# Optimization experiments

Hardware: AMD Instinct MI355X
Metric: run time of the kernel (lower is better)

The kernel has to match this reference:

```python
import jax, jax.numpy as jnp
import numpy as np

V, E, H, B, S = 32000, 128, 256, 8, 512


def setup_inputs() -> dict:
    key = jax.random.key(0)
    ks = jax.random.split(key, 8)
    s_cell = 1.0 / np.sqrt(H)
    return {
        "t": jax.random.randint(ks[0], (B, S), 0, V),
        "emb": jax.random.normal(ks[1], (V, E), dtype=jnp.float32) * 0.02,
        "h0": jnp.zeros((1, H), dtype=jnp.float32),
        "w_ih": jax.random.uniform(ks[2], (3 * H, E), jnp.float32, -s_cell, s_cell),
        "w_hh": jax.random.uniform(ks[3], (3 * H, H), jnp.float32, -s_cell, s_cell),
        "b_ih": jax.random.uniform(ks[4], (3 * H,), jnp.float32, -s_cell, s_cell),
        "b_hh": jax.random.uniform(ks[5], (3 * H,), jnp.float32, -s_cell, s_cell),
        "w_out": jax.random.normal(ks[6], (V, H), dtype=jnp.float32) * 0.02,
        "b_out": jnp.zeros((V,), dtype=jnp.float32),
    }


def reference(t, emb, h0, w_ih, w_hh, b_ih, b_hh, w_out, b_out):
    x = emb[t]  # [B, S, E]
    # Input-side gate pre-activations can be batched over time (same math as per-step GRUCell)
    gi = jnp.einsum("bse,ge->bsg", x, w_ih) + b_ih  # [B, S, 3H]
    h_init = jnp.broadcast_to(h0, (t.shape[0], h0.shape[1]))  # [B, H]

    def step(h, gi_t):  # gi_t: [B, 3H]
        gh = h @ w_hh.T + b_hh  # [B, 3H]
        i_r, i_z, i_n = jnp.split(gi_t, 3, axis=-1)
        h_r, h_z, h_n = jnp.split(gh, 3, axis=-1)
        r = jax.nn.sigmoid(i_r + h_r)
        z = jax.nn.sigmoid(i_z + h_z)
        n = jnp.tanh(i_n + r * h_n)
        h_new = (1.0 - z) * n + z * h
        return h_new, h_new

    _, hs = jax.lax.scan(step, h_init, jnp.swapaxes(gi, 0, 1))  # hs: [S, B, H]
    hidden = jnp.swapaxes(hs, 0, 1)  # [B, S, H]
    return jnp.einsum("bsh,vh->bsv", hidden, w_out) + b_out  # [B, S, V]
```

## Files before the change

kernel.cpp:

```cpp
#include <hip/hip_runtime.h>
#include <stdint.h>


typedef __attribute__((ext_vector_type(8))) _Float16 half8;
typedef __attribute__((ext_vector_type(4))) _Float16 half4;
typedef __attribute__((ext_vector_type(4))) float float4v;
typedef __attribute__((ext_vector_type(4))) float facc4;
typedef __attribute__((ext_vector_type(4))) unsigned short ushort4v;

#define GI_BYTES   (512 * 8 * 768 * 4)
#define HID_BYTES  (4096 * 256 * 2)
#define FLAG_OFF   (GI_BYTES + HID_BYTES)

__device__ __forceinline__ float b2f(unsigned short u) {
  union { unsigned int i; float f; } v; v.i = ((unsigned int)u) << 16; return v.f;
}
__device__ __forceinline__ unsigned short f2b(float f) {
  union { float f; unsigned int i; } v; v.f = f;
  unsigned int r = v.i + 0x7FFFu + ((v.i >> 16) & 1u);
  return (unsigned short)(r >> 16);
}
template<bool BF> __device__ __forceinline__ float ldf(const void* p, int i) {
  if constexpr (BF) return b2f(((const unsigned short*)p)[i]);
  else              return ((const float*)p)[i];
}
template<bool BF> __device__ __forceinline__ float4v ld4(const void* p, int i) {
  float4v r;
  if constexpr (BF) {
    ushort4v u = *reinterpret_cast<const ushort4v*>((const unsigned short*)p + i);
#pragma unroll
    for (int j = 0; j < 4; ++j) r[j] = b2f(u[j]);
  } else {
    r = *reinterpret_cast<const float4v*>((const float*)p + i);
  }
  return r;
}

__global__ void k_detect(const unsigned int* __restrict__ emb_raw,
                         int* __restrict__ flag) {
  int tid = threadIdx.x;
  unsigned int u = emb_raw[tid];
  unsigned int lo = u & 0xFFFFu;
  unsigned int ex = (lo >> 7) & 0xFFu;
  int hit = ((ex >= 96u && ex <= 127u) || lo == 0u) ? 1 : 0;
  unsigned long long m = __ballot(hit);
  if (tid == 0) flag[0] = (__popcll(m) >= 40) ? 1 : 0;
}

template<bool BF>
__global__ __launch_bounds__(256, 4) void k_gi(
    const int* __restrict__ flag, const int* __restrict__ t,
    const void* __restrict__ emb, const void* __restrict__ w_ih,
    const void* __restrict__ b_ih, float* __restrict__ gi)
{
  if (*flag != (BF ? 1 : 0)) return;
  alignas(16) __shared__ float x_lds[4][128];
  const int n0 = blockIdx.x * 4;
  const int tid = threadIdx.x;
  for (int i = tid; i < 512; i += 256) {
    int tk = i >> 7, e = i & 127;
    int n = n0 + tk, s = n >> 3, b = n & 7;
    int tok = t[b * 512 + s];
    x_lds[tk][e] = ldf<BF>(emb, tok * 128 + e);
  }
  __syncthreads();
#pragma unroll
  for (int gg = 0; gg < 3; ++gg) {
    int g = gg * 256 + tid;
    float bias = ldf<BF>(b_ih, g);
    float a0 = bias, a1 = bias, a2 = bias, a3 = bias;
    for (int kb = 0; kb < 32; ++kb) {
      float4v w4 = ld4<BF>(w_ih, g * 128 + kb * 4);
#pragma unroll
      for (int j = 0; j < 4; ++j) {
        float w = w4[j]; int k = kb * 4 + j;
        a0 = fmaf(w, x_lds[0][k], a0);
        a1 = fmaf(w, x_lds[1][k], a1);
        a2 = fmaf(w, x_lds[2][k], a2);
        a3 = fmaf(w, x_lds[3][k], a3);
      }
    }
    gi[(n0 + 0) * 768 + g] = a0;
    gi[(n0 + 1) * 768 + g] = a1;
    gi[(n0 + 2) * 768 + g] = a2;
    gi[(n0 + 3) * 768 + g] = a3;
  }
}

template<bool BF>
__global__ __launch_bounds__(512, 2) void k_scan(
    const int* __restrict__ flag, const void* __restrict__ w_hh,
    const void* __restrict__ b_hh, const void* __restrict__ h0,
    const float* __restrict__ gi, _Float16* __restrict__ hidden)
{
  if (*flag != (BF ? 1 : 0)) return;
  alignas(16) __shared__ _Float16 a_lds[4096];
  alignas(16) __shared__ float gh_lds[8 * 772];
  alignas(16) __shared__ float bhh_lds[768];

  const int tid = threadIdx.x;
  const int wave = tid >> 6, lane = tid & 63;
  const int l15 = lane & 15, q = lane >> 4;
  const int b = tid & 7, jb = tid >> 3, j0 = jb * 4;
  const int kt0 = jb >> 3, q0 = (jb >> 1) & 3, off0 = (jb & 1) * 4;

  half8 bfr[6][8];
#pragma unroll
  for (int tt = 0; tt < 6; ++tt) {
    int nrow = wave * 96 + tt * 16 + l15;
#pragma unroll
    for (int kt = 0; kt < 8; ++kt) {
      int base = nrow * 256 + kt * 32 + q * 8;
      float4v x0 = ld4<BF>(w_hh, base), x1 = ld4<BF>(w_hh, base + 4);
      half8 h;
#pragma unroll
      for (int j = 0; j < 4; ++j) { h[j] = (_Float16)x0[j]; h[4 + j] = (_Float16)x1[j]; }
      bfr[tt][kt] = h;
    }
  }

  for (int i = tid; i < 4096; i += 512) a_lds[i] = (_Float16)0.f;
  for (int i = tid; i < 768; i += 512) bhh_lds[i] = ldf<BF>(b_hh, i);
  __syncthreads();

  float hreg[4];
  {
    float4v h04 = ld4<BF>(h0, j0);
    half4 h4;
#pragma unroll
    for (int i = 0; i < 4; ++i) { hreg[i] = h04[i]; h4[i] = (_Float16)h04[i]; }
    *reinterpret_cast<half4*>(&a_lds[kt0 * 512 + (q0 * 16 + b) * 8 + off0]) = h4;
  }
  __syncthreads();

  for (int s = 0; s < 512; ++s) {
    facc4 acc[6] = {};
#pragma unroll
    for (int kt = 0; kt < 8; ++kt) {
      half8 a = *reinterpret_cast<const half8*>(&a_lds[kt * 512 + lane * 8]);
#pragma unroll
      for (int tt = 0; tt < 6; ++tt)
        acc[tt] = __builtin_amdgcn_mfma_f32_16x16x32_f16(a, bfr[tt][kt],
                                                         acc[tt], 0, 0, 0);
    }
    const float* gis = gi + s * 6144 + b * 768 + j0;
    float4v g_r = *reinterpret_cast<const float4v*>(gis);
    float4v g_z = *reinterpret_cast<const float4v*>(gis + 256);
    float4v g_n = *reinterpret_cast<const float4v*>(gis + 512);
    if (q < 2) {
#pragma unroll
      for (int tt = 0; tt < 6; ++tt) {
        int nrow = wave * 96 + tt * 16 + l15;
#pragma unroll
        for (int i = 0; i < 4; ++i)
          gh_lds[(q * 4 + i) * 772 + nrow] = acc[tt][i] + bhh_lds[nrow];
      }
    }
    __syncthreads();

    const float* ghb = gh_lds + b * 772;
    half4 hb;
#pragma unroll
    for (int i = 0; i < 4; ++i) {
      int j = j0 + i;
      float r = 1.f / (1.f + __expf(-(g_r[i] + ghb[j])));
      float z = 1.f / (1.f + __expf(-(g_z[i] + ghb[256 + j])));
      float xn = g_n[i] + r * ghb[512 + j];
      float e2 = __expf(2.f * xn);
      float nn = 1.f - 2.f / (e2 + 1.f);
      float hnew = (1.f - z) * nn + z * hreg[i];
      hreg[i] = hnew;
      hb[i] = (_Float16)hnew;
    }
    *reinterpret_cast<half4*>(&a_lds[kt0 * 512 + (q0 * 16 + b) * 8 + off0]) = hb;
    *reinterpret_cast<half4*>(hidden + (b * 512 + s) * 256 + j0) = hb;
    __syncthreads();
  }
}

template<bool BF>
__global__ __launch_bounds__(256, 2) void k_out(
    const int* __restrict__ flag, const _Float16* __restrict__ hidden,
    const void* __restrict__ w_out, const void* __restrict__ b_out,
    void* __restrict__ out)
{
  if (*flag != (BF ? 1 : 0)) return;
  alignas(16) __shared__ _Float16 Asm[128 * 72];
  alignas(16) __shared__ _Float16 Bsm[128 * 72];
  const int bid = blockIdx.x;
  const int m0 = (bid & 31) * 128;
  const int n0 = (bid >> 5) * 128;
  const int tid = threadIdx.x;
  const int wave = tid >> 6, lane = tid & 63;
  const int l15 = lane & 15, q = lane >> 4;
  const int wm = (wave >> 1) * 64, wn = (wave & 1) * 64;

  facc4 acc[4][4] = {};
  float bo[4];
#pragma unroll
  for (int nt = 0; nt < 4; ++nt)
    bo[nt] = ldf<BF>(b_out, n0 + wn + nt * 16 + l15);

  for (int kk = 0; kk < 4; ++kk) {
    int k0 = kk * 64;
#pragma unroll
    for (int r = 0; r < 4; ++r) {
      int row = r * 32 + (tid >> 3);
      int ch = tid & 7;
      *reinterpret_cast<half8*>(&Asm[row * 72 + ch * 8]) =
          *reinterpret_cast<const half8*>(hidden + (m0 + row) * 256 + k0 + ch * 8);
      int wbase = (n0 + row) * 256 + k0 + ch * 8;
      float4v w0 = ld4<BF>(w_out, wbase), w1 = ld4<BF>(w_out, wbase + 4);
      half8 hB;
#pragma unroll
      for (int j = 0; j < 4; ++j) { hB[j] = (_Float16)w0[j]; hB[4 + j] = (_Float16)w1[j]; }
      *reinterpret_cast<half8*>(&Bsm[row * 72 + ch * 8]) = hB;
    }
    __syncthreads();
#pragma unroll
    for (int kt = 0; kt < 2; ++kt) {
      int koff = kt * 32 + q * 8;
      half8 af[4], bf[4];
#pragma unroll
      for (int mt = 0; mt < 4; ++mt)
        af[mt] = *reinterpret_cast<const half8*>(&Asm[(wm + mt * 16 + l15) * 72 + koff]);
#pragma unroll
      for (int nt = 0; nt < 4; ++nt)
        bf[nt] = *reinterpret_cast<const half8*>(&Bsm[(wn + nt * 16 + l15) * 72 + koff]);
#pragma unroll
      for (int mt = 0; mt < 4; ++mt)
#pragma unroll
        for (int nt = 0; nt < 4; ++nt)
          acc[mt][nt] = __builtin_amdgcn_mfma_f32_16x16x32_f16(
              af[mt], bf[nt], acc[mt][nt], 0, 0, 0);
    }
    __syncthreads();
  }
#pragma unroll
  for (int mt = 0; mt < 4; ++mt) {
#pragma unroll
    for (int i = 0; i < 4; ++i) {
      int row = m0 + wm + mt * 16 + q * 4 + i;
#pragma unroll
      for (int nt = 0; nt < 4; ++nt) {
        int col = n0 + wn + nt * 16 + l15;
        float val = acc[mt][nt][i] + bo[nt];
        if constexpr (BF) ((unsigned short*)out)[row * 32000 + col] = f2b(val);
        else              ((float*)out)[row * 32000 + col] = val;
      }
    }
  }
}

extern "C" void kernel_launch(void* const* d_in, const int* in_sizes, int n_in,
                              void* d_out, int out_size, void* d_ws, size_t ws_size,
                              hipStream_t stream) {
  const int* t     = (const int*)d_in[0];
  const void* emb  = d_in[1];
  const void* h0   = d_in[2];
  const void* w_ih = d_in[3];
  const void* w_hh = d_in[4];
  const void* b_ih = d_in[5];
  const void* b_hh = d_in[6];
  const void* w_out = d_in[7];
  const void* b_out = d_in[8];

  float*     gi     = (float*)d_ws;
  _Float16*  hidden = (_Float16*)((char*)d_ws + GI_BYTES);
  int*       flag   = (int*)((char*)d_ws + FLAG_OFF);

  k_detect<<<1, 64, 0, stream>>>((const unsigned int*)emb, flag);

  k_gi<false><<<1024, 256, 0, stream>>>(flag, t, emb, w_ih, b_ih, gi);
  k_gi<true> <<<1024, 256, 0, stream>>>(flag, t, emb, w_ih, b_ih, gi);

  k_scan<false><<<1, 512, 0, stream>>>(flag, w_hh, b_hh, h0, gi, hidden);
  k_scan<true> <<<1, 512, 0, stream>>>(flag, w_hh, b_hh, h0, gi, hidden);

  k_out<false><<<8000, 256, 0, stream>>>(flag, hidden, w_out, b_out, d_out);
  k_out<true> <<<8000, 256, 0, stream>>>(flag, hidden, w_out, b_out, d_out);
}
```

Before: 1.795 ms.

## Split GRU scan across batch blocks with one sync per step

```diff
diff --git a/kernel.cpp b/kernel.cpp
--- a/kernel.cpp
+++ b/kernel.cpp
@@ -88,93 +88,89 @@
 }
 
 template<bool BF>
-__global__ __launch_bounds__(512, 2) void k_scan(
+__global__ __launch_bounds__(1024, 4) void k_scan(
     const int* __restrict__ flag, const void* __restrict__ w_hh,
     const void* __restrict__ b_hh, const void* __restrict__ h0,
     const float* __restrict__ gi, _Float16* __restrict__ hidden)
 {
   if (*flag != (BF ? 1 : 0)) return;
-  alignas(16) __shared__ _Float16 a_lds[4096];
-  alignas(16) __shared__ float gh_lds[8 * 772];
-  alignas(16) __shared__ float bhh_lds[768];
+  alignas(16) __shared__ _Float16 a_sh[2][256];
+  alignas(16) __shared__ float gi_sh[2][768];
+  alignas(16) __shared__ float bhh_sh[768];
 
   const int tid = threadIdx.x;
+  const int b = blockIdx.x;
   const int wave = tid >> 6, lane = tid & 63;
   const int l15 = lane & 15, q = lane >> 4;
-  const int b = tid & 7, jb = tid >> 3, j0 = jb * 4;
-  const int kt0 = jb >> 3, q0 = (jb >> 1) & 3, off0 = (jb & 1) * 4;
-
-  half8 bfr[6][8];
-#pragma unroll
-  for (int tt = 0; tt < 6; ++tt) {
-    int nrow = wave * 96 + tt * 16 + l15;
+  const bool ard = (l15 == 0);
+  const int qo = q * 8;
+
+  half8 bfr[3][8];
+#pragma unroll
+  for (int tt = 0; tt < 3; ++tt) {
+    int nrow = tt * 256 + (wave << 4) + l15;
 #pragma unroll
     for (int kt = 0; kt < 8; ++kt) {
-      int base = nrow * 256 + kt * 32 + q * 8;
+      int base = nrow * 256 + kt * 32 + qo;
       float4v x0 = ld4<BF>(w_hh, base), x1 = ld4<BF>(w_hh, base + 4);
       half8 h;
 #pragma unroll
-      for (int j = 0; j < 4; ++j) { h[j] = (_Float16)x0[j]; h[4 + j] = (_Float16)x1[j]; }
+      for (int jj = 0; jj < 4; ++jj) { h[jj] = (_Float16)x0[jj]; h[4 + jj] = (_Float16)x1[jj]; }
       bfr[tt][kt] = h;
     }
   }
 
-  for (int i = tid; i < 4096; i += 512) a_lds[i] = (_Float16)0.f;
-  for (int i = tid; i < 768; i += 512) bhh_lds[i] = ldf<BF>(b_hh, i);
+  if (tid < 768) bhh_sh[tid] = ldf<BF>(b_hh, tid);
+  if (tid < 256) a_sh[0][tid] = (_Float16)ldf<BF>(h0, tid);
+  if (tid < 768) gi_sh[0][tid] = gi[b * 768 + tid];
+  float hreg = 0.f;
+  if (lane < 16) hreg = ldf<BF>(h0, (wave << 4) + lane);
+
+  half8 a0 = {}, a1 = {};
+  _Float16* hid = hidden + b * 512 * 256;
   __syncthreads();
 
-  float hreg[4];
-  {
-    float4v h04 = ld4<BF>(h0, j0);
-    half4 h4;
-#pragma unroll
-    for (int i = 0; i < 4; ++i) { hreg[i] = h04[i]; h4[i] = (_Float16)h04[i]; }
-    *reinterpret_cast<half4*>(&a_lds[kt0 * 512 + (q0 * 16 + b) * 8 + off0]) = h4;
-  }
-  __syncthreads();
-
+  int p = 0;
   for (int s = 0; s < 512; ++s) {
-    facc4 acc[6] = {};
-#pragma unroll
-    for (int kt = 0; kt < 8; ++kt) {
-      half8 a = *reinterpret_cast<const half8*>(&a_lds[kt * 512 + lane * 8]);
-#pragma unroll
-      for (int tt = 0; tt < 6; ++tt)
-        acc[tt] = __builtin_amdgcn_mfma_f32_16x16x32_f16(a, bfr[tt][kt],
-                                                         acc[tt], 0, 0, 0);
-    }
-    const float* gis = gi + s * 6144 + b * 768 + j0;
-    float4v g_r = *reinterpret_cast<const float4v*>(gis);
-    float4v g_z = *reinterpret_cast<const float4v*>(gis + 256);
-    float4v g_n = *reinterpret_cast<const float4v*>(gis + 512);
-    if (q < 2) {
-#pragma unroll
-      for (int tt = 0; tt < 6; ++tt) {
-        int nrow = wave * 96 + tt * 16 + l15;
-#pragma unroll
-        for (int i = 0; i < 4; ++i)
-          gh_lds[(q * 4 + i) * 772 + nrow] = acc[tt][i] + bhh_lds[nrow];
-      }
-    }
-    __syncthreads();
-
-    const float* ghb = gh_lds + b * 772;
-    half4 hb;
-#pragma unroll
-    for (int i = 0; i < 4; ++i) {
-      int j = j0 + i;
-      float r = 1.f / (1.f + __expf(-(g_r[i] + ghb[j])));
-      float z = 1.f / (1.f + __expf(-(g_z[i] + ghb[256 + j])));
-      float xn = g_n[i] + r * ghb[512 + j];
+    float gnext = 0.f;
+    if (tid < 768 && s < 511) gnext = gi[(s + 1) * 6144 + b * 768 + tid];
+
+    const _Float16* ap = &a_sh[p][0];
+    facc4 acc0 = {}, acc1 = {}, acc2 = {};
+    if (ard) a0 = *reinterpret_cast<const half8*>(ap + qo);
+#pragma unroll
+    for (int kt = 0; kt < 8; kt += 2) {
+      if (ard) a1 = *reinterpret_cast<const half8*>(ap + (kt + 1) * 32 + qo);
+      acc0 = __builtin_amdgcn_mfma_f32_16x16x32_f16(a0, bfr[0][kt], acc0, 0, 0, 0);
+      acc1 = __builtin_amdgcn_mfma_f32_16x16x32_f16(a0, bfr[1][kt], acc1, 0, 0, 0);
+      acc2 = __builtin_amdgcn_mfma_f32_16x16x32_f16(a0, bfr[2][kt], acc2, 0, 0, 0);
+      if (ard && kt + 2 < 8) a0 = *reinterpret_cast<const half8*>(ap + (kt + 2) * 32 + qo);
+      acc0 = __builtin_amdgcn_mfma_f32_16x16x32_f16(a1, bfr[0][kt + 1], acc0, 0, 0, 0);
+      acc1 = __builtin_amdgcn_mfma_f32_16x16x32_f16(a1, bfr[1][kt + 1], acc1, 0, 0, 0);
+      acc2 = __builtin_amdgcn_mfma_f32_16x16x32_f16(a1, bfr[2][kt + 1], acc2, 0, 0, 0);
+    }
+
+    if (tid < 768 && s < 511) gi_sh[p ^ 1][tid] = gnext;
+
+    if (lane < 16) {
+      int j = (wave << 4) + lane;
+      float ghr = acc0[0] + bhh_sh[j];
+      float ghz = acc1[0] + bhh_sh[256 + j];
+      float ghn = acc2[0] + bhh_sh[512 + j];
+      float gir = gi_sh[p][j], giz = gi_sh[p][256 + j], gin = gi_sh[p][512 + j];
+      float r = 1.f / (1.f + __expf(-(gir + ghr)));
+      float z = 1.f / (1.f + __expf(-(giz + ghz)));
+      float xn = gin + r * ghn;
       float e2 = __expf(2.f * xn);
       float nn = 1.f - 2.f / (e2 + 1.f);
-      float hnew = (1.f - z) * nn + z * hreg[i];
-      hreg[i] = hnew;
-      hb[i] = (_Float16)hnew;
-    }
-    *reinterpret_cast<half4*>(&a_lds[kt0 * 512 + (q0 * 16 + b) * 8 + off0]) = hb;
-    *reinterpret_cast<half4*>(hidden + (b * 512 + s) * 256 + j0) = hb;
+      float hnew = (1.f - z) * nn + z * hreg;
+      hreg = hnew;
+      _Float16 hf = (_Float16)hnew;
+      a_sh[p ^ 1][j] = hf;
+      hid[s * 256 + j] = hf;
+    }
     __syncthreads();
+    p ^= 1;
   }
 }
 
@@ -274,8 +270,8 @@
   k_gi<false><<<1024, 256, 0, stream>>>(flag, t, emb, w_ih, b_ih, gi);
   k_gi<true> <<<1024, 256, 0, stream>>>(flag, t, emb, w_ih, b_ih, gi);
 
-  k_scan<false><<<1, 512, 0, stream>>>(flag, w_hh, b_hh, h0, gi, hidden);
-  k_scan<true> <<<1, 512, 0, stream>>>(flag, w_hh, b_hh, h0, gi, hidden);
+  k_scan<false><<<8, 1024, 0, stream>>>(flag, w_hh, b_hh, h0, gi, hidden);
+  k_scan<true> <<<8, 1024, 0, stream>>>(flag, w_hh, b_hh, h0, gi, hidden);
 
   k_out<false><<<8000, 256, 0, stream>>>(flag, hidden, w_out, b_out, d_out);
   k_out<true> <<<8000, 256, 0, stream>>>(flag, hidden, w_out, b_out, d_out);
```

New measurement: 1.533 ms. -14.6%, faster.
